# Optimization experiments

Measured on AMD Instinct MI355X. Metric: run time of the kernel, lower is better.

Reference implementation:

```python
import jax, jax.numpy as jnp
import numpy as np

D_MODEL = 1024
NUM_HEADS = 16
HEAD_DIM = D_MODEL // NUM_HEADS
B, S = 2, 2048


def setup_inputs() -> dict:
    key = jax.random.key(0)
    ks = jax.random.split(key, 6)
    scale = 0.02
    return {
        "x": jax.random.normal(ks[0], (B, S, D_MODEL), dtype=jnp.float32),
        "mask": jax.random.normal(ks[1], (S, S), dtype=jnp.float32),
        "Wqkv": jax.random.normal(ks[2], (D_MODEL, 3 * D_MODEL), dtype=jnp.float32) * scale,
        "bqkv": jax.random.normal(ks[3], (3 * D_MODEL,), dtype=jnp.float32) * scale,
        "Wout": jax.random.normal(ks[4], (D_MODEL, D_MODEL), dtype=jnp.float32) * scale,
        "bout": jax.random.normal(ks[5], (D_MODEL,), dtype=jnp.float32) * scale,
    }


def reference(x, mask, Wqkv, bqkv, Wout, bout):
    b, s, d = x.shape
    h, hd = NUM_HEADS, HEAD_DIM
    qkv = x @ Wqkv + bqkv                              # [b, s, 3d]
    qkv = qkv.reshape(b, s, h, 3 * hd).transpose(0, 2, 1, 3)  # [b, h, s, 3hd]
    q, k, v = jnp.split(qkv, 3, axis=-1)               # each [b, h, s, hd]
    scaled = jnp.einsum("bhqd,bhkd->bhqk", q, k) / jnp.sqrt(jnp.float32(hd))
    scaled = scaled + mask                             # mask [s, s] broadcasts
    attn = jax.nn.softmax(scaled, axis=-1)
    values = jnp.einsum("bhqk,bhkd->bhqd", attn, v)    # [b, h, s, hd]
    values = values.transpose(0, 2, 1, 3).reshape(b, s, d)
    return values @ Wout + bout
```

## Files before the change

### kernel.cpp

```cpp
#include <hip/hip_runtime.h>
#include <hip/hip_bf16.h>

#define D_MODEL 1024
#define NH 16
#define HD 64
#define BATCH 2
#define SEQ 2048
#define M_TOTAL (BATCH*SEQ)

typedef _Float16 f16;
typedef _Float16 half8 __attribute__((ext_vector_type(8)));
typedef _Float16 half4v __attribute__((ext_vector_type(4)));
typedef float floatx4 __attribute__((ext_vector_type(4)));

__device__ inline void gload_lds16(const void* g, void* l) {
    __builtin_amdgcn_global_load_lds(
        (const __attribute__((address_space(1))) unsigned int*)g,
        (__attribute__((address_space(3))) unsigned int*)l, 16, 0, 0);
}

__global__ void cvt_f32_f16(const float* __restrict__ src, f16* __restrict__ dst, int n4) {
    int i = blockIdx.x * blockDim.x + threadIdx.x;
    if (i < n4) {
        float4 v = ((const float4*)src)[i];
        half4v o = { (f16)v.x, (f16)v.y, (f16)v.z, (f16)v.w };
        *(half4v*)(dst + (long)i * 4) = o;
    }
}

__global__ void exp_cvt(const float* __restrict__ src, f16* __restrict__ dst, int n4) {
    int i = blockIdx.x * blockDim.x + threadIdx.x;
    if (i < n4) {
        float4 v = ((const float4*)src)[i];
        half4v o = { (f16)__expf(v.x), (f16)__expf(v.y), (f16)__expf(v.z), (f16)__expf(v.w) };
        *(half4v*)(dst + (long)i * 4) = o;
    }
}

__global__ void transpose_cvt(const float* __restrict__ src, f16* __restrict__ dst, int R, int C) {
    __shared__ float tile[32][33];
    int tx = threadIdx.x;
    int ty = threadIdx.y;
    int c0 = blockIdx.x * 32;
    int r0 = blockIdx.y * 32;
    for (int yy = 0; yy < 32; yy += 8)
        tile[ty + yy][tx] = src[(long)(r0 + ty + yy) * C + c0 + tx];
    __syncthreads();
    for (int yy = 0; yy < 32; yy += 8)
        dst[(long)(c0 + ty + yy) * R + r0 + tx] = (f16)tile[tx][ty + yy];
}

template<int MODE, int TN>
__global__ __launch_bounds__(256) void gemm_mfma(
    const f16* __restrict__ A, const f16* __restrict__ BT,
    const float* __restrict__ bias,
    f16* __restrict__ Qh, f16* __restrict__ Kh, f16* __restrict__ Vtg,
    float* __restrict__ out, int Kdim)
{
    constexpr int NF = TN / 32;
    __shared__ f16 Ah[128 * 64];
    __shared__ f16 Bh[TN * 64];
    int tid  = threadIdx.x;
    int wid  = tid >> 6;
    int lane = tid & 63;
    int quad = lane >> 4;
    int l16  = lane & 15;
    int m0 = blockIdx.y * 128;
    int n0 = blockIdx.x * TN;
    int mrow = (wid >> 1) * 64;
    int ncol = (wid & 1) * (TN / 2);
    int grow = lane >> 3;
    int gchunk = (lane & 7) ^ (grow & 7);
    int sw0 = ((quad)     ^ (l16 & 7)) * 8;
    int sw1 = ((quad + 4) ^ (l16 & 7)) * 8;

    floatx4 acc[4][NF];
    #pragma unroll
    for (int mb = 0; mb < 4; mb++)
        #pragma unroll
        for (int nb = 0; nb < NF; nb++) acc[mb][nb] = (floatx4){0.f, 0.f, 0.f, 0.f};

    const f16* Abase = A + (long)m0 * Kdim;
    const f16* Bbase = BT + (long)n0 * Kdim;

    for (int k0 = 0; k0 < Kdim; k0 += 64) {
        #pragma unroll
        for (int j = 0; j < 4; j++) {
            int r = j * 32 + wid * 8 + grow;
            gload_lds16(Abase + (long)r * Kdim + k0 + gchunk * 8, &Ah[(j * 32 + wid * 8) * 64]);
        }
        #pragma unroll
        for (int j = 0; j < TN / 32; j++) {
            int r = j * 32 + wid * 8 + grow;
            gload_lds16(Bbase + (long)r * Kdim + k0 + gchunk * 8, &Bh[(j * 32 + wid * 8) * 64]);
        }
        __syncthreads();
        #pragma unroll
        for (int h = 0; h < 2; h++) {
            int sw = h ? sw1 : sw0;
            half8 af[4];
            #pragma unroll
            for (int mb = 0; mb < 4; mb++)
                af[mb] = *(const half8*)&Ah[(mrow + mb * 16 + l16) * 64 + sw];
            #pragma unroll
            for (int nb = 0; nb < NF; nb++) {
                half8 bf = *(const half8*)&Bh[(ncol + nb * 16 + l16) * 64 + sw];
                #pragma unroll
                for (int mb = 0; mb < 4; mb++)
                    acc[mb][nb] = __builtin_amdgcn_mfma_f32_16x16x32_f16(af[mb], bf, acc[mb][nb], 0, 0, 0);
            }
        }
        __syncthreads();
    }

    #pragma unroll
    for (int nb = 0; nb < NF; nb++) {
        int n = n0 + ncol + nb * 16 + l16;
        float bv = bias[n];
        int head = 0, t = 0, d = 0;
        if (MODE == 0) { head = n / 192; int rem = n % 192; t = rem / 64; d = rem % 64; }
        #pragma unroll
        for (int mb = 0; mb < 4; mb++) {
            int mbase = m0 + mrow + mb * 16 + quad * 4;
            if (MODE == 0) {
                int b = mbase >> 11;
                int s = mbase & 2047;
                long bh = b * NH + head;
                if (t == 2) {
                    half4v pack;
                    #pragma unroll
                    for (int r = 0; r < 4; r++) pack[r] = (f16)(acc[mb][nb][r] + bv);
                    *(half4v*)&Vtg[(bh * HD + d) * SEQ + s] = pack;
                } else if (t == 0) {
                    #pragma unroll
                    for (int r = 0; r < 4; r++)
                        Qh[(bh * SEQ + s + r) * HD + d] = (f16)((acc[mb][nb][r] + bv) * 0.125f);
                } else {
                    #pragma unroll
                    for (int r = 0; r < 4; r++)
                        Kh[(bh * SEQ + s + r) * HD + d] = (f16)(acc[mb][nb][r] + bv);
                }
            } else {
                #pragma unroll
                for (int r = 0; r < 4; r++)
                    out[(long)(mbase + r) * D_MODEL + n] = acc[mb][nb][r] + bv;
            }
        }
    }
}

__global__ __launch_bounds__(256) void attn(
    const f16* __restrict__ Qh, const f16* __restrict__ Kh, const f16* __restrict__ Vtg,
    const f16* __restrict__ E, f16* __restrict__ valh)
{
    __shared__ f16 Kl[64 * 64];
    __shared__ f16 Vt[64 * 64];
    __shared__ f16 Pl[4][32 * 68];
    int tid  = threadIdx.x;
    int wid  = tid >> 6;
    int lane = tid & 63;
    int quad = lane >> 4;
    int l16  = lane & 15;
    int bh = blockIdx.y;
    int b  = bh >> 4;
    int h  = bh & 15;
    int q0 = blockIdx.x * 128 + wid * 32;

    int grow = lane >> 3;
    int gchunk = (lane & 7) ^ (grow & 7);
    int sw0 = ((quad)     ^ (l16 & 7)) * 8;
    int sw1 = ((quad + 4) ^ (l16 & 7)) * 8;

    const f16* Qbase = Qh + ((long)bh * SEQ + q0) * HD;
    half8 qf[2][2];
    #pragma unroll
    for (int m = 0; m < 2; m++)
        #pragma unroll
        for (int c = 0; c < 2; c++)
            qf[m][c] = *(const half8*)&Qbase[(long)(m * 16 + l16) * HD + c * 32 + quad * 8];

    floatx4 Of[2][4];
    float sums[2][4];
    #pragma unroll
    for (int m = 0; m < 2; m++) {
        #pragma unroll
        for (int nb = 0; nb < 4; nb++) Of[m][nb] = (floatx4){0.f, 0.f, 0.f, 0.f};
        #pragma unroll
        for (int r = 0; r < 4; r++) sums[m][r] = 0.f;
    }

    const f16* Kb = Kh + (long)bh * SEQ * HD;
    const f16* Vb = Vtg + (long)bh * HD * SEQ;

    for (int k0 = 0; k0 < SEQ; k0 += 64) {
        __syncthreads();
        #pragma unroll
        for (int j = 0; j < 2; j++) {
            int r = j * 32 + wid * 8 + grow;
            gload_lds16(Kb + (long)(k0 + r) * HD + gchunk * 8, &Kl[(j * 32 + wid * 8) * 64]);
            gload_lds16(Vb + (long)r * SEQ + k0 + gchunk * 8, &Vt[(j * 32 + wid * 8) * 64]);
        }
        __syncthreads();

        f16 ef[2][4][4];
        #pragma unroll
        for (int m = 0; m < 2; m++)
            #pragma unroll
            for (int r = 0; r < 4; r++) {
                const f16* Erow = E + (long)(q0 + m * 16 + quad * 4 + r) * SEQ + k0 + l16;
                #pragma unroll
                for (int kb = 0; kb < 4; kb++) ef[m][r][kb] = Erow[kb * 16];
            }

        floatx4 sc[2][4];
        #pragma unroll
        for (int kb = 0; kb < 4; kb++) {
            half8 kf0 = *(const half8*)&Kl[(kb * 16 + l16) * 64 + sw0];
            half8 kf1 = *(const half8*)&Kl[(kb * 16 + l16) * 64 + sw1];
            #pragma unroll
            for (int m = 0; m < 2; m++) {
                floatx4 s = (floatx4){0.f, 0.f, 0.f, 0.f};
                s = __builtin_amdgcn_mfma_f32_16x16x32_f16(qf[m][0], kf0, s, 0, 0, 0);
                s = __builtin_amdgcn_mfma_f32_16x16x32_f16(qf[m][1], kf1, s, 0, 0, 0);
                sc[m][kb] = s;
            }
        }

        #pragma unroll
        for (int m = 0; m < 2; m++)
            #pragma unroll
            for (int kb = 0; kb < 4; kb++)
                #pragma unroll
                for (int r = 0; r < 4; r++) {
                    float p = (float)ef[m][r][kb] * __expf(sc[m][kb][r]);
                    sums[m][r] += p;
                    Pl[wid][(m * 16 + quad * 4 + r) * 68 + kb * 16 + l16] = (f16)p;
                }

        half8 pf[2][2];
        #pragma unroll
        for (int m = 0; m < 2; m++)
            #pragma unroll
            for (int c = 0; c < 2; c++)
                pf[m][c] = *(const half8*)&Pl[wid][(m * 16 + l16) * 68 + c * 32 + quad * 8];

        #pragma unroll
        for (int nb = 0; nb < 4; nb++) {
            half8 vf0 = *(const half8*)&Vt[(nb * 16 + l16) * 64 + sw0];
            half8 vf1 = *(const half8*)&Vt[(nb * 16 + l16) * 64 + sw1];
            #pragma unroll
            for (int m = 0; m < 2; m++) {
                Of[m][nb] = __builtin_amdgcn_mfma_f32_16x16x32_f16(pf[m][0], vf0, Of[m][nb], 0, 0, 0);
                Of[m][nb] = __builtin_amdgcn_mfma_f32_16x16x32_f16(pf[m][1], vf1, Of[m][nb], 0, 0, 0);
            }
        }
    }

    #pragma unroll
    for (int m = 0; m < 2; m++)
        #pragma unroll
        for (int r = 0; r < 4; r++) {
            float s = sums[m][r];
            s += __shfl_xor(s, 1);
            s += __shfl_xor(s, 2);
            s += __shfl_xor(s, 4);
            s += __shfl_xor(s, 8);
            sums[m][r] = 1.f / s;
        }

    #pragma unroll
    for (int m = 0; m < 2; m++)
        #pragma unroll
        for (int nb = 0; nb < 4; nb++)
            #pragma unroll
            for (int r = 0; r < 4; r++) {
                int q = q0 + m * 16 + quad * 4 + r;
                int d = nb * 16 + l16;
                valh[((long)(b * SEQ + q)) * D_MODEL + h * HD + d] = (f16)(Of[m][nb][r] * sums[m][r]);
            }
}

extern "C" void kernel_launch(void* const* d_in, const int* in_sizes, int n_in,
                              void* d_out, int out_size, void* d_ws, size_t ws_size,
                              hipStream_t stream) {
    const float* x    = (const float*)d_in[0];
    const float* mask = (const float*)d_in[1];
    const float* Wqkv = (const float*)d_in[2];
    const float* bqkv = (const float*)d_in[3];
    const float* Wout = (const float*)d_in[4];
    const float* bout = (const float*)d_in[5];
    float* out = (float*)d_out;

    char* ws = (char*)d_ws;
    f16* xh    = (f16*)(ws + 0);
    f16* E     = (f16*)(ws + 0);
    f16* WqkvT = (f16*)(ws + 8388608);
    f16* WoutT = (f16*)(ws + 14680064);
    f16* Qh    = (f16*)(ws + 16777216);
    f16* Kh    = (f16*)(ws + 25165824);
    f16* Vtg   = (f16*)(ws + 33554432);
    f16* valh  = (f16*)(ws + 41943040);

    cvt_f32_f16<<<4096, 256, 0, stream>>>(x, xh, M_TOTAL * D_MODEL / 4);
    transpose_cvt<<<dim3(96, 32), dim3(32, 8), 0, stream>>>(Wqkv, WqkvT, 1024, 3072);
    transpose_cvt<<<dim3(32, 32), dim3(32, 8), 0, stream>>>(Wout, WoutT, 1024, 1024);
    gemm_mfma<0, 128><<<dim3(24, 32), 256, 0, stream>>>(xh, WqkvT, bqkv, Qh, Kh, Vtg, nullptr, 1024);
    exp_cvt<<<4096, 256, 0, stream>>>(mask, E, SEQ * SEQ / 4);
    attn<<<dim3(16, 32), 256, 0, stream>>>(Qh, Kh, Vtg, E, valh);
    gemm_mfma<1, 64><<<dim3(16, 32), 256, 0, stream>>>(valh, WoutT, bout, nullptr, nullptr, nullptr, out, 1024);
}
```

Baseline: 227.5 us.

## Double-buffer attention K/V, use exp2 with folded log2e, XCD-aware block remap

The attention kernel now double-buffers K/V tiles in LDS, so the next tile loads while the current one is computed, and it drops one barrier per iteration. Softmax switches to exp2: log2e is folded into the Q scale and the mask preconversion, and the row sums are computed with an MFMA against a ones vector instead of adds plus shuffles. Both GEMMs and the attention kernel remap block IDs so tiles that share data land on the same XCD, which should improve L2 reuse. s_setprio hints are added around the MFMA sections. The cost is more LDS per block and extra MFMA work for the row sums. Unnormalised exp without a running max carries the same overflow risk as the old code.

Result: faster. 222.8 us (-2.1%).

```diff
diff --git a/kernel.cpp b/kernel.cpp
--- a/kernel.cpp
+++ b/kernel.cpp
@@ -13,6 +13,12 @@
 typedef _Float16 half4v __attribute__((ext_vector_type(4)));
 typedef float floatx4 __attribute__((ext_vector_type(4)));
 
+#if __has_builtin(__builtin_amdgcn_exp2f)
+#define EXP2(x) __builtin_amdgcn_exp2f(x)
+#else
+#define EXP2(x) __expf(0.6931471805599453f * (x))
+#endif
+
 __device__ inline void gload_lds16(const void* g, void* l) {
     __builtin_amdgcn_global_load_lds(
         (const __attribute__((address_space(1))) unsigned int*)g,
@@ -28,11 +34,12 @@
     }
 }
 
-__global__ void exp_cvt(const float* __restrict__ src, f16* __restrict__ dst, int n4) {
+__global__ void l2scale_cvt(const float* __restrict__ src, f16* __restrict__ dst, int n4) {
     int i = blockIdx.x * blockDim.x + threadIdx.x;
     if (i < n4) {
         float4 v = ((const float4*)src)[i];
-        half4v o = { (f16)__expf(v.x), (f16)__expf(v.y), (f16)__expf(v.z), (f16)__expf(v.w) };
+        const float L2E = 1.44269504f;
+        half4v o = { (f16)(v.x * L2E), (f16)(v.y * L2E), (f16)(v.z * L2E), (f16)(v.w * L2E) };
         *(half4v*)(dst + (long)i * 4) = o;
     }
 }
@@ -65,8 +72,14 @@
     int lane = tid & 63;
     int quad = lane >> 4;
     int l16  = lane & 15;
-    int m0 = blockIdx.y * 128;
-    int n0 = blockIdx.x * TN;
+
+    int id  = blockIdx.y * gridDim.x + blockIdx.x;
+    int xcd = id & 7;
+    int s   = id >> 3;
+    constexpr int CN = (MODE == 0) ? 12 : 8;
+    int n0 = ((xcd & 1) * CN + s % CN) * TN;
+    int m0 = ((xcd >> 1) * 8 + s / CN) * 128;
+
     int mrow = (wid >> 1) * 64;
     int ncol = (wid & 1) * (TN / 2);
     int grow = lane >> 3;
@@ -124,21 +137,21 @@
             int mbase = m0 + mrow + mb * 16 + quad * 4;
             if (MODE == 0) {
                 int b = mbase >> 11;
-                int s = mbase & 2047;
+                int ss = mbase & 2047;
                 long bh = b * NH + head;
                 if (t == 2) {
                     half4v pack;
                     #pragma unroll
                     for (int r = 0; r < 4; r++) pack[r] = (f16)(acc[mb][nb][r] + bv);
-                    *(half4v*)&Vtg[(bh * HD + d) * SEQ + s] = pack;
+                    *(half4v*)&Vtg[(bh * HD + d) * SEQ + ss] = pack;
                 } else if (t == 0) {
                     #pragma unroll
                     for (int r = 0; r < 4; r++)
-                        Qh[(bh * SEQ + s + r) * HD + d] = (f16)((acc[mb][nb][r] + bv) * 0.125f);
+                        Qh[(bh * SEQ + ss + r) * HD + d] = (f16)((acc[mb][nb][r] + bv) * 0.18033688f);
                 } else {
                     #pragma unroll
                     for (int r = 0; r < 4; r++)
-                        Kh[(bh * SEQ + s + r) * HD + d] = (f16)(acc[mb][nb][r] + bv);
+                        Kh[(bh * SEQ + ss + r) * HD + d] = (f16)(acc[mb][nb][r] + bv);
                 }
             } else {
                 #pragma unroll
@@ -153,18 +166,24 @@
     const f16* __restrict__ Qh, const f16* __restrict__ Kh, const f16* __restrict__ Vtg,
     const f16* __restrict__ E, f16* __restrict__ valh)
 {
-    __shared__ f16 Kl[64 * 64];
-    __shared__ f16 Vt[64 * 64];
+    __shared__ f16 Kl[2][64 * 64];
+    __shared__ f16 Vt[2][64 * 64];
     __shared__ f16 Pl[4][32 * 68];
     int tid  = threadIdx.x;
     int wid  = tid >> 6;
     int lane = tid & 63;
     int quad = lane >> 4;
     int l16  = lane & 15;
-    int bh = blockIdx.y;
+
+    int id   = blockIdx.y * 16 + blockIdx.x;
+    int xcd  = id & 7;
+    int slot = id >> 3;
+    int bh   = ((xcd & 3) << 3) | (slot >> 3);
+    int qx   = ((xcd >> 2) << 3) | (slot & 7);
     int b  = bh >> 4;
     int h  = bh & 15;
-    int q0 = blockIdx.x * 128 + wid * 32;
+    int qblk = qx * 128;
+    int q0 = qblk + wid * 32;
 
     int grow = lane >> 3;
     int gchunk = (lane & 7) ^ (grow & 7);
@@ -179,52 +198,64 @@
         for (int c = 0; c < 2; c++)
             qf[m][c] = *(const half8*)&Qbase[(long)(m * 16 + l16) * HD + c * 32 + quad * 8];
 
+    half8 onesv;
+    #pragma unroll
+    for (int j = 0; j < 8; j++) onesv[j] = (f16)1.0f;
+
     floatx4 Of[2][4];
-    float sums[2][4];
+    floatx4 ssum[2];
     #pragma unroll
     for (int m = 0; m < 2; m++) {
+        ssum[m] = (floatx4){0.f, 0.f, 0.f, 0.f};
         #pragma unroll
         for (int nb = 0; nb < 4; nb++) Of[m][nb] = (floatx4){0.f, 0.f, 0.f, 0.f};
-        #pragma unroll
-        for (int r = 0; r < 4; r++) sums[m][r] = 0.f;
     }
 
     const f16* Kb = Kh + (long)bh * SEQ * HD;
     const f16* Vb = Vtg + (long)bh * HD * SEQ;
-
-    for (int k0 = 0; k0 < SEQ; k0 += 64) {
-        __syncthreads();
+    const f16* Eb = E + (long)qblk * SEQ;
+
+    auto stage = [&](int buf, int k0) {
         #pragma unroll
         for (int j = 0; j < 2; j++) {
             int r = j * 32 + wid * 8 + grow;
-            gload_lds16(Kb + (long)(k0 + r) * HD + gchunk * 8, &Kl[(j * 32 + wid * 8) * 64]);
-            gload_lds16(Vb + (long)r * SEQ + k0 + gchunk * 8, &Vt[(j * 32 + wid * 8) * 64]);
-        }
-        __syncthreads();
+            gload_lds16(Kb + (long)(k0 + r) * HD + gchunk * 8, &Kl[buf][(j * 32 + wid * 8) * 64]);
+            gload_lds16(Vb + (long)r * SEQ + k0 + gchunk * 8, &Vt[buf][(j * 32 + wid * 8) * 64]);
+        }
+    };
+
+    stage(0, 0);
+    __syncthreads();
+
+    auto iter = [&](const int buf, int k0) {
+        bool notlast = (k0 + 64 < SEQ);
+        if (notlast) stage(buf ^ 1, k0 + 64);
 
         f16 ef[2][4][4];
         #pragma unroll
         for (int m = 0; m < 2; m++)
             #pragma unroll
             for (int r = 0; r < 4; r++) {
-                const f16* Erow = E + (long)(q0 + m * 16 + quad * 4 + r) * SEQ + k0 + l16;
+                const f16* Erow = Eb + (long)(wid * 32 + m * 16 + quad * 4 + r) * SEQ + k0 + l16;
                 #pragma unroll
                 for (int kb = 0; kb < 4; kb++) ef[m][r][kb] = Erow[kb * 16];
             }
 
         floatx4 sc[2][4];
+        __builtin_amdgcn_s_setprio(1);
         #pragma unroll
         for (int kb = 0; kb < 4; kb++) {
-            half8 kf0 = *(const half8*)&Kl[(kb * 16 + l16) * 64 + sw0];
-            half8 kf1 = *(const half8*)&Kl[(kb * 16 + l16) * 64 + sw1];
+            half8 kf0 = *(const half8*)&Kl[buf][(kb * 16 + l16) * 64 + sw0];
+            half8 kf1 = *(const half8*)&Kl[buf][(kb * 16 + l16) * 64 + sw1];
             #pragma unroll
             for (int m = 0; m < 2; m++) {
-                floatx4 s = (floatx4){0.f, 0.f, 0.f, 0.f};
-                s = __builtin_amdgcn_mfma_f32_16x16x32_f16(qf[m][0], kf0, s, 0, 0, 0);
-                s = __builtin_amdgcn_mfma_f32_16x16x32_f16(qf[m][1], kf1, s, 0, 0, 0);
-                sc[m][kb] = s;
-            }
-        }
+                floatx4 sacc = (floatx4){0.f, 0.f, 0.f, 0.f};
+                sacc = __builtin_amdgcn_mfma_f32_16x16x32_f16(qf[m][0], kf0, sacc, 0, 0, 0);
+                sacc = __builtin_amdgcn_mfma_f32_16x16x32_f16(qf[m][1], kf1, sacc, 0, 0, 0);
+                sc[m][kb] = sacc;
+            }
+        }
+        __builtin_amdgcn_s_setprio(0);
 
         #pragma unroll
         for (int m = 0; m < 2; m++)
@@ -232,8 +263,7 @@
             for (int kb = 0; kb < 4; kb++)
                 #pragma unroll
                 for (int r = 0; r < 4; r++) {
-                    float p = (float)ef[m][r][kb] * __expf(sc[m][kb][r]);
-                    sums[m][r] += p;
+                    float p = EXP2(sc[m][kb][r] + (float)ef[m][r][kb]);
                     Pl[wid][(m * 16 + quad * 4 + r) * 68 + kb * 16 + l16] = (f16)p;
                 }
 
@@ -244,29 +274,37 @@
             for (int c = 0; c < 2; c++)
                 pf[m][c] = *(const half8*)&Pl[wid][(m * 16 + l16) * 68 + c * 32 + quad * 8];
 
+        __builtin_amdgcn_s_setprio(1);
+        #pragma unroll
+        for (int m = 0; m < 2; m++) {
+            ssum[m] = __builtin_amdgcn_mfma_f32_16x16x32_f16(pf[m][0], onesv, ssum[m], 0, 0, 0);
+            ssum[m] = __builtin_amdgcn_mfma_f32_16x16x32_f16(pf[m][1], onesv, ssum[m], 0, 0, 0);
+        }
         #pragma unroll
         for (int nb = 0; nb < 4; nb++) {
-            half8 vf0 = *(const half8*)&Vt[(nb * 16 + l16) * 64 + sw0];
-            half8 vf1 = *(const half8*)&Vt[(nb * 16 + l16) * 64 + sw1];
+            half8 vf0 = *(const half8*)&Vt[buf][(nb * 16 + l16) * 64 + sw0];
+            half8 vf1 = *(const half8*)&Vt[buf][(nb * 16 + l16) * 64 + sw1];
             #pragma unroll
             for (int m = 0; m < 2; m++) {
                 Of[m][nb] = __builtin_amdgcn_mfma_f32_16x16x32_f16(pf[m][0], vf0, Of[m][nb], 0, 0, 0);
                 Of[m][nb] = __builtin_amdgcn_mfma_f32_16x16x32_f16(pf[m][1], vf1, Of[m][nb], 0, 0, 0);
             }
         }
-    }
-
+        __builtin_amdgcn_s_setprio(0);
+
+        __syncthreads();
+    };
+
+    for (int k0 = 0; k0 < SEQ; k0 += 128) {
+        iter(0, k0);
+        iter(1, k0 + 64);
+    }
+
+    float rinv[2][4];
     #pragma unroll
     for (int m = 0; m < 2; m++)
         #pragma unroll
-        for (int r = 0; r < 4; r++) {
-            float s = sums[m][r];
-            s += __shfl_xor(s, 1);
-            s += __shfl_xor(s, 2);
-            s += __shfl_xor(s, 4);
-            s += __shfl_xor(s, 8);
-            sums[m][r] = 1.f / s;
-        }
+        for (int r = 0; r < 4; r++) rinv[m][r] = 1.f / ssum[m][r];
 
     #pragma unroll
     for (int m = 0; m < 2; m++)
@@ -276,7 +314,7 @@
             for (int r = 0; r < 4; r++) {
                 int q = q0 + m * 16 + quad * 4 + r;
                 int d = nb * 16 + l16;
-                valh[((long)(b * SEQ + q)) * D_MODEL + h * HD + d] = (f16)(Of[m][nb][r] * sums[m][r]);
+                valh[((long)(b * SEQ + q)) * D_MODEL + h * HD + d] = (f16)(Of[m][nb][r] * rinv[m][r]);
             }
 }
 
@@ -305,7 +343,7 @@
     transpose_cvt<<<dim3(96, 32), dim3(32, 8), 0, stream>>>(Wqkv, WqkvT, 1024, 3072);
     transpose_cvt<<<dim3(32, 32), dim3(32, 8), 0, stream>>>(Wout, WoutT, 1024, 1024);
     gemm_mfma<0, 128><<<dim3(24, 32), 256, 0, stream>>>(xh, WqkvT, bqkv, Qh, Kh, Vtg, nullptr, 1024);
-    exp_cvt<<<4096, 256, 0, stream>>>(mask, E, SEQ * SEQ / 4);
+    l2scale_cvt<<<4096, 256, 0, stream>>>(mask, E, SEQ * SEQ / 4);
     attn<<<dim3(16, 32), 256, 0, stream>>>(Qh, Kh, Vtg, E, valh);
     gemm_mfma<1, 64><<<dim3(16, 32), 256, 0, stream>>>(valh, WoutT, bout, nullptr, nullptr, nullptr, out, 1024);
 }
```
